# Optimization experiments

Measured on AMD Instinct MI355X. Metric: run time of the kernel, lower is better.

The kernel has to match this reference:

```python
import jax, jax.numpy as jnp
import numpy as np

B, H, N, D, BD, K = 8, 8, 65536, 128, 64, 32


def _l2norm(x, eps=1e-12):
    n = jnp.linalg.norm(x, axis=-1, keepdims=True)
    return x / jnp.maximum(n, eps)


def _topk_sparse_softmax(sim, k):
    # softmax over the top-k entries per (b,h); zeros elsewhere (== masked_fill -inf softmax)
    vals, idx = jax.lax.top_k(sim, k)              # [B,H,k]
    wk = jax.nn.softmax(vals, axis=-1)
    b = jnp.arange(sim.shape[0])[:, None, None]
    h = jnp.arange(sim.shape[1])[None, :, None]
    return jnp.zeros_like(sim).at[b, h, idx].set(wk)  # [B,H,N]


def setup_inputs() -> dict:
    key = jax.random.key(0)
    ks = jax.random.split(key, 14)
    return {
        "memory": jax.random.normal(ks[0], (B, N, D), jnp.float32),
        "read_keys": jax.random.normal(ks[1], (B, H, D), jnp.float32),
        "write_keys": jax.random.normal(ks[2], (B, H, D), jnp.float32),
        "write_vals": jax.random.normal(ks[3], (B, H, D), jnp.float32),
        "erase": jax.random.uniform(ks[4], (B, H), jnp.float32),
        "add_gate": jax.random.uniform(ks[5], (B, H), jnp.float32),
        "beta_r": jax.random.uniform(ks[6], (B, H), jnp.float32),
        "beta_w": jax.random.uniform(ks[7], (B, H), jnp.float32),
        "W_b1": jax.random.normal(ks[8], (D, BD), jnp.float32) * 0.02,
        "b_b1": jnp.zeros((BD,), jnp.float32),
        "W_b2": jax.random.normal(ks[9], (BD, D), jnp.float32) * 0.02,
        "b_b2": jnp.zeros((D,), jnp.float32),
        "W_merge": jax.random.normal(ks[10], (H * D, D), jnp.float32) * 0.02,
        "b_merge": jnp.zeros((D,), jnp.float32),
        "ln_g": jnp.ones((D,), jnp.float32),
        "ln_b": jnp.zeros((D,), jnp.float32),
        "decay_gate": jnp.ones((N,), jnp.float32) * 0.99,
    }


def reference(memory, read_keys, write_keys, write_vals, erase, add_gate,
              beta_r, beta_w, W_b1, b_b1, W_b2, b_b2, W_merge, b_merge,
              ln_g, ln_b, decay_gate):
    # ---- write (erase/add with top-k addressing, head-mean, normalize, decay) ----
    cvals = jax.nn.gelu(write_vals @ W_b1 + b_b1, approximate=False) @ W_b2 + b_b2  # [B,H,D]
    sim_w = jnp.einsum('bhd,bnd->bhn', _l2norm(write_keys), _l2norm(memory)) * beta_w[..., None]
    ww = _topk_sparse_softmax(sim_w, K)                                # [B,H,N]
    # mean_h[mem*(1-w*e)] = mem*(1-mean_h(w*e));  mean_h[w*add*cvals] via einsum/H
    erase_mean = (ww * erase[..., None]).mean(axis=1)                  # [B,N]
    add_part = jnp.einsum('bhn,bhd->bnd', ww * add_gate[..., None], cvals) / H
    mem2 = memory * (1.0 - erase_mean)[..., None] + add_part
    mem2 = _l2norm(mem2 + 1e-8)
    mem2 = mem2 * jax.nn.sigmoid(decay_gate)[None, :, None]            # decay gate

    # ---- read (from updated memory) ----
    sim_r = jnp.einsum('bhd,bnd->bhn', _l2norm(read_keys), _l2norm(mem2)) * beta_r[..., None]
    wr = _topk_sparse_softmax(sim_r, K)
    rph = jnp.einsum('bhn,bnd->bhd', wr, mem2).reshape(mem2.shape[0], H * D)
    merged = rph @ W_merge + b_merge                                   # [B,D]
    mu = merged.mean(axis=-1, keepdims=True)
    var = jnp.mean((merged - mu) ** 2, axis=-1, keepdims=True)
    out = (merged - mu) / jnp.sqrt(var + 1e-5) * ln_g + ln_b           # LayerNorm
    return out
```

## Files before the change

kernel.cpp:

```cpp
#include <hip/hip_runtime.h>
#include <hip/hip_bf16.h>

#define BB   8
#define HH   8
#define NN   65536
#define DD   128
#define BDIM 64
#define KK   32


#define OFF_SIMW 0u
#define OFF_SIMR (OFF_SIMW + 4194304u)
#define OFF_NWK  (OFF_SIMR + 4194304u)
#define OFF_NRK  (OFF_NWK + 8192u)
#define OFF_CV   (OFF_NRK + 8192u)
#define OFF_WIDX (OFF_CV + 8192u)
#define OFF_WVAL (OFF_WIDX + 2048u)
#define OFF_RIDX (OFF_WVAL + 2048u)
#define OFF_RVAL (OFF_RIDX + 2048u)
#define OFF_M2U  (OFF_RVAL + 2048u)
#define OFF_RPH  (OFF_M2U + 262144u)

__device__ __forceinline__ float brsum128(float v, float* sred, int tid) {
  #pragma unroll
  for (int o = 32; o > 0; o >>= 1) v += __shfl_xor(v, o);
  __syncthreads();
  if ((tid & 63) == 0) sred[tid >> 6] = v;
  __syncthreads();
  return sred[0] + sred[1];
}

__global__ __launch_bounds__(128) void k1_setup(
    const float* __restrict__ wkeys, const float* __restrict__ rkeys,
    const float* __restrict__ wvals,
    const float* __restrict__ beta_r, const float* __restrict__ beta_w,
    const float* __restrict__ W_b1, const float* __restrict__ b_b1,
    const float* __restrict__ W_b2, const float* __restrict__ b_b2,
    float* __restrict__ nwk, float* __restrict__ nrk,
    float* __restrict__ cvals, float* __restrict__ rph) {
  int g = blockIdx.x;
  int d = threadIdx.x;
  __shared__ float sred[2];
  __shared__ float wv_s[DD];
  __shared__ float hid[BDIM];

  rph[g * DD + d] = 0.f;

  float wk = wkeys[g * DD + d];
  float rk = rkeys[g * DD + d];
  float wv = wvals[g * DD + d];
  wv_s[d] = wv;

  float s = brsum128(wk * wk, sred, d);
  nwk[g * DD + d] = wk / fmaxf(sqrtf(s), 1e-12f) * beta_w[g];
  s = brsum128(rk * rk, sred, d);
  nrk[g * DD + d] = rk / fmaxf(sqrtf(s), 1e-12f) * beta_r[g];

  __syncthreads();
  if (d < BDIM) {
    float a = b_b1[d];
    #pragma unroll 4
    for (int dd = 0; dd < DD; ++dd) a += wv_s[dd] * W_b1[dd * BDIM + d];
    hid[d] = a * 0.5f * (1.f + erff(a * 0.70710678118654752f));
  }
  __syncthreads();
  float c = b_b2[d];
  #pragma unroll 4
  for (int j = 0; j < BDIM; ++j) c += hid[j] * W_b2[j * DD + d];
  cvals[g * DD + d] = c;
}

__global__ __launch_bounds__(256) void k2_sims(
    const float* __restrict__ mem,
    const float* __restrict__ nwk, const float* __restrict__ nrk,
    float* __restrict__ simw, float* __restrict__ simr) {
  int blk = blockIdx.x;
  int b   = blk >> 8;
  int n   = ((blk & 255) << 8) + threadIdx.x;
  const float4* rowp = (const float4*)(mem + ((size_t)b * NN + n) * DD);

  float dw[HH] = {0,0,0,0,0,0,0,0};
  float dr[HH] = {0,0,0,0,0,0,0,0};
  float nw = 0.f, nr = 0.f;
  const float* kw = nwk + b * HH * DD;
  const float* kr = nrk + b * HH * DD;

  for (int g = 0; g < 4; ++g) {
    float4 q[8];
    #pragma unroll
    for (int i = 0; i < 8; ++i) q[i] = rowp[g * 8 + i];
    #pragma unroll
    for (int i = 0; i < 8; ++i) {
      float xs[4] = {q[i].x, q[i].y, q[i].z, q[i].w};
      #pragma unroll
      for (int e = 0; e < 4; ++e) {
        float xv = xs[e];
        float xr = xv + 1e-8f;
        nw += xv * xv;
        nr += xr * xr;
        int d = g * 32 + i * 4 + e;
        #pragma unroll
        for (int h = 0; h < HH; ++h) {
          dw[h] += xv * kw[h * DD + d];
          dr[h] += xr * kr[h * DD + d];
        }
      }
    }
  }
  float riw = 1.f / fmaxf(sqrtf(nw), 1e-12f);
  float rir = 1.f / fmaxf(sqrtf(nr), 1e-12f);
  #pragma unroll
  for (int h = 0; h < HH; ++h) {
    simw[(size_t)(b * HH + h) * NN + n] = dw[h] * riw;
    simr[(size_t)(b * HH + h) * NN + n] = dr[h] * rir;
  }
}

#define NBKT 1024
#define MAXC 4096
__global__ __launch_bounds__(256) void k_topk(
    const float* __restrict__ sims, int* __restrict__ oidx, float* __restrict__ oval) {
  int blk = blockIdx.x;
  int tid = threadIdx.x;
  const float*  s  = sims + (size_t)blk * NN;
  const float4* s4 = (const float4*)s;
  __shared__ float redv[256];
  __shared__ unsigned hist[NBKT];
  __shared__ float cv[MAXC];
  __shared__ int   ci[MAXC];
  __shared__ float sM, sm, sscale;
  __shared__ int   sthr, scnt;
  __shared__ float selv[KK];
  __shared__ int   seli[KK];

  float mx = -1e30f, mn = 1e30f;
  #pragma unroll 4
  for (int i = tid; i < NN / 4; i += 256) {
    float4 v = s4[i];
    mx = fmaxf(mx, fmaxf(fmaxf(v.x, v.y), fmaxf(v.z, v.w)));
    mn = fminf(mn, fminf(fminf(v.x, v.y), fminf(v.z, v.w)));
  }
  redv[tid] = mx; __syncthreads();
  for (int st = 128; st > 0; st >>= 1) { if (tid < st) redv[tid] = fmaxf(redv[tid], redv[tid + st]); __syncthreads(); }
  if (tid == 0) sM = redv[0];
  __syncthreads();
  redv[tid] = mn; __syncthreads();
  for (int st = 128; st > 0; st >>= 1) { if (tid < st) redv[tid] = fminf(redv[tid], redv[tid + st]); __syncthreads(); }
  if (tid == 0) {
    sm = redv[0];
    float r = sM - sm;
    sscale = (r > 0.f) ? ((float)NBKT / r) : 0.f;
    scnt = 0;
  }
  for (int i = tid; i < NBKT; i += 256) hist[i] = 0u;
  __syncthreads();

  float m_ = sm, sc_ = sscale;
  #pragma unroll 2
  for (int i = tid; i < NN / 4; i += 256) {
    float4 v = s4[i];
    float xs[4] = {v.x, v.y, v.z, v.w};
    #pragma unroll
    for (int e = 0; e < 4; ++e) {
      int bkt = (int)((xs[e] - m_) * sc_);
      bkt = min(NBKT - 1, max(0, bkt));
      atomicAdd(&hist[bkt], 1u);
    }
  }
  __syncthreads();
  if (tid == 0) {
    unsigned acc = 0; int t = NBKT - 1;
    for (; t >= 0; --t) { acc += hist[t]; if (acc >= KK) break; }
    sthr = (t < 0) ? 0 : t;
  }
  __syncthreads();

  int thr = sthr;
  #pragma unroll 2
  for (int i = tid; i < NN / 4; i += 256) {
    float4 v = s4[i];
    float xs[4] = {v.x, v.y, v.z, v.w};
    #pragma unroll
    for (int e = 0; e < 4; ++e) {
      float vv = xs[e];
      int bkt = (int)((vv - m_) * sc_);
      bkt = min(NBKT - 1, max(0, bkt));
      if (bkt >= thr) {
        int p = atomicAdd(&scnt, 1);
        if (p < MAXC) { cv[p] = vv; ci[p] = i * 4 + e; }
      }
    }
  }
  __syncthreads();
  int nc = min(scnt, MAXC);

  if (tid < 64) {
    for (int k = 0; k < KK; ++k) {
      unsigned long long best = 0ull, lbest = 0ull;
      int lj = -1;
      for (int j = tid; j < nc; j += 64) {
        float v = cv[j];
        unsigned u = __float_as_uint(v);
        u = (u & 0x80000000u) ? ~u : (u | 0x80000000u);
        unsigned long long key = ((unsigned long long)u << 32) | (unsigned)(~(unsigned)ci[j]);
        if (key > lbest) { lbest = key; lj = j; }
      }
      best = lbest;
      #pragma unroll
      for (int o = 32; o > 0; o >>= 1) {
        unsigned long long t = __shfl_xor(best, o);
        if (t > best) best = t;
      }
      if (lbest == best && lj >= 0) cv[lj] = -1e30f;
      if (tid == 0) {
        unsigned u = (unsigned)(best >> 32);
        float v = (u & 0x80000000u) ? __uint_as_float(u & 0x7fffffffu) : __uint_as_float(~u);
        selv[k] = v;
        seli[k] = (int)~(unsigned)(best & 0xffffffffu);
      }
    }
    if (tid == 0) {
      float m0 = selv[0], ssum = 0.f;
      float es[KK];
      #pragma unroll
      for (int k = 0; k < KK; ++k) { es[k] = expf(selv[k] - m0); ssum += es[k]; }
      float inv = 1.f / ssum;
      #pragma unroll
      for (int k = 0; k < KK; ++k) {
        oidx[blk * KK + k] = seli[k];
        oval[blk * KK + k] = es[k] * inv;
      }
    }
  }
}

__global__ __launch_bounds__(128) void k4_write(
    const float* __restrict__ mem, const float* __restrict__ erase,
    const float* __restrict__ adg,
    const int* __restrict__ widx, const float* __restrict__ wval,
    const float* __restrict__ cvals, const float* __restrict__ nrk,
    float* __restrict__ mem2u, float* __restrict__ simr) {
  int b  = blockIdx.x >> 8;
  int sl = blockIdx.x & 255;
  int d  = threadIdx.x;
  __shared__ int   swi[256];
  __shared__ float swv[256];
  __shared__ float sred[2 * 9];

  swi[d]       = widx[b * 256 + d];
  swi[d + 128] = widx[b * 256 + d + 128];
  swv[d]       = wval[b * 256 + d];
  swv[d + 128] = wval[b * 256 + d + 128];
  __syncthreads();

  int n = swi[sl];
  for (int j = 0; j < sl; ++j) if (swi[j] == n) return;

  float E = 0.f, addd = 0.f;
  #pragma unroll
  for (int h = 0; h < HH; ++h) {
    float er = erase[b * HH + h];
    float ag = adg[b * HH + h];
    float aw = 0.f;
    #pragma unroll 4
    for (int k = 0; k < KK; ++k) {
      int j = h * KK + k;
      if (swi[j] == n) { float wv = swv[j]; E += wv * er; aw += wv; }
    }
    addd += aw * ag * cvals[(b * HH + h) * DD + d];
  }
  float mval = mem[((size_t)b * NN + n) * DD + d];
  float v = mval * (1.f - E * 0.125f) + addd * 0.125f + 1e-8f;

  float r[9];
  r[0] = v * v;
  #pragma unroll
  for (int h = 0; h < HH; ++h) r[1 + h] = nrk[(b * HH + h) * DD + d] * v;
  #pragma unroll
  for (int o = 32; o > 0; o >>= 1) {
    #pragma unroll
    for (int i = 0; i < 9; ++i) r[i] += __shfl_xor(r[i], o);
  }
  if ((d & 63) == 0) {
    int w = d >> 6;
    #pragma unroll
    for (int i = 0; i < 9; ++i) sred[w * 9 + i] = r[i];
  }
  __syncthreads();
  float S    = sred[0] + sred[9];
  float rinv = 1.f / fmaxf(sqrtf(S), 1e-12f);
  mem2u[(size_t)(b * 256 + sl) * DD + d] = v * rinv;
  if (d < HH) simr[(size_t)(b * HH + d) * NN + n] = (sred[1 + d] + sred[9 + 1 + d]) * rinv;
}

__global__ __launch_bounds__(128) void k6_gather(
    const float* __restrict__ mem, const float* __restrict__ decay,
    const int* __restrict__ widx, const int* __restrict__ ridx,
    const float* __restrict__ rval, const float* __restrict__ mem2u,
    float* __restrict__ rph) {
  int b   = blockIdx.x >> 8;
  int rem = blockIdx.x & 255;
  int d   = threadIdx.x;
  __shared__ int swi[256];
  __shared__ float sred[2];
  swi[d]       = widx[b * 256 + d];
  swi[d + 128] = widx[b * 256 + d + 128];
  __syncthreads();

  int n   = ridx[b * HH * KK + rem];
  float w = rval[b * HH * KK + rem];
  float sc = 1.f / (1.f + expf(-decay[n]));
  int slot = -1;
  for (int j = 0; j < 256; ++j) if (swi[j] == n) { slot = j; break; }
  float u;
  if (slot >= 0) {
    u = mem2u[(size_t)(b * 256 + slot) * DD + d];
  } else {
    float v = mem[((size_t)b * NN + n) * DD + d] + 1e-8f;
    float S = brsum128(v * v, sred, d);
    u = v / fmaxf(sqrtf(S), 1e-12f);
  }
  int h = rem >> 5;
  atomicAdd(&rph[(b * HH + h) * DD + d], w * sc * u);
}

__global__ __launch_bounds__(512) void k7_merge(
    const float* __restrict__ rph, const float* __restrict__ W_merge,
    const float* __restrict__ b_merge, const float* __restrict__ ln_g,
    const float* __restrict__ ln_b, float* __restrict__ out) {
  int b = blockIdx.x;
  int tid = threadIdx.x;
  int d = tid & 127;
  int p = tid >> 7;
  __shared__ float acc_s[4][DD];
  __shared__ float accf[DD];
  __shared__ float smu, svar;

  float a = 0.f;
  int j0 = p * 256;
  #pragma unroll 4
  for (int j = j0; j < j0 + 256; ++j)
    a += rph[b * HH * DD + j] * W_merge[j * DD + d];
  acc_s[p][d] = a;
  __syncthreads();
  if (tid < DD) accf[d] = b_merge[d] + acc_s[0][d] + acc_s[1][d] + acc_s[2][d] + acc_s[3][d];
  __syncthreads();
  if (tid < 64) {
    float x0 = accf[tid], x1 = accf[tid + 64];
    float s1 = x0 + x1, s2 = x0 * x0 + x1 * x1;
    #pragma unroll
    for (int o = 32; o > 0; o >>= 1) { s1 += __shfl_xor(s1, o); s2 += __shfl_xor(s2, o); }
    if (tid == 0) { smu = s1 * (1.f / DD); svar = s2 * (1.f / DD) - smu * smu; }
  }
  __syncthreads();
  if (tid < DD)
    out[b * DD + d] = (accf[d] - smu) * rsqrtf(svar + 1e-5f) * ln_g[d] + ln_b[d];
}

extern "C" void kernel_launch(void* const* d_in, const int* in_sizes, int n_in,
                              void* d_out, int out_size, void* d_ws, size_t ws_size,
                              hipStream_t stream) {
  const float* memory  = (const float*)d_in[0];
  const float* rkeys   = (const float*)d_in[1];
  const float* wkeys   = (const float*)d_in[2];
  const float* wvals   = (const float*)d_in[3];
  const float* erase   = (const float*)d_in[4];
  const float* adg     = (const float*)d_in[5];
  const float* beta_r  = (const float*)d_in[6];
  const float* beta_w  = (const float*)d_in[7];
  const float* W_b1    = (const float*)d_in[8];
  const float* b_b1    = (const float*)d_in[9];
  const float* W_b2    = (const float*)d_in[10];
  const float* b_b2    = (const float*)d_in[11];
  const float* W_merge = (const float*)d_in[12];
  const float* b_merge = (const float*)d_in[13];
  const float* ln_g    = (const float*)d_in[14];
  const float* ln_b    = (const float*)d_in[15];
  const float* decay   = (const float*)d_in[16];

  float* ws   = (float*)d_ws;
  float* simw = ws + OFF_SIMW;
  float* simr = ws + OFF_SIMR;
  float* nwk  = ws + OFF_NWK;
  float* nrk  = ws + OFF_NRK;
  float* cv   = ws + OFF_CV;
  int*   widx = (int*)(ws + OFF_WIDX);
  float* wval = ws + OFF_WVAL;
  int*   ridx = (int*)(ws + OFF_RIDX);
  float* rval = ws + OFF_RVAL;
  float* m2u  = ws + OFF_M2U;
  float* rph  = ws + OFF_RPH;

  hipLaunchKernelGGL(k1_setup, dim3(BB * HH), dim3(128), 0, stream,
                     wkeys, rkeys, wvals, beta_r, beta_w, W_b1, b_b1, W_b2, b_b2,
                     nwk, nrk, cv, rph);
  hipLaunchKernelGGL(k2_sims, dim3(BB * (NN / 256)), dim3(256), 0, stream,
                     memory, nwk, nrk, simw, simr);
  hipLaunchKernelGGL(k_topk, dim3(BB * HH), dim3(256), 0, stream, simw, widx, wval);
  hipLaunchKernelGGL(k4_write, dim3(BB * 256), dim3(128), 0, stream,
                     memory, erase, adg, widx, wval, cv, nrk, m2u, simr);
  hipLaunchKernelGGL(k_topk, dim3(BB * HH), dim3(256), 0, stream, simr, ridx, rval);
  hipLaunchKernelGGL(k6_gather, dim3(BB * 256), dim3(128), 0, stream,
                     memory, decay, widx, ridx, rval, m2u, rph);
  hipLaunchKernelGGL(k7_merge, dim3(BB), dim3(512), 0, stream,
                     rph, W_merge, b_merge, ln_g, ln_b, (float*)d_out);
}
```

Measured before the change: 628.6 us.

## Replace single-block histogram top-k with two-stage parallel wave-level top-k

The old top-k ran one block per (b,h) row: it scanned 65536 scores three times with shared-memory histogram atomics, then did a serial selection. It becomes two kernels. Stage 1 splits each row over 16 blocks of 4 waves, and each wave picks its local top-32 from 1024 register-held keys by repeated shuffle-max. Stage 2 merges the 2048 candidates per row in one wave and computes the softmax with lane shuffles. This spreads work across far more CUs and removes the atomic histogram passes, at the cost of an extra launch and a small candidate buffer.

```diff
diff --git a/kernel.cpp b/kernel.cpp
--- a/kernel.cpp
+++ b/kernel.cpp
@@ -20,6 +20,16 @@
 #define OFF_RVAL (OFF_RIDX + 2048u)
 #define OFF_M2U  (OFF_RVAL + 2048u)
 #define OFF_RPH  (OFF_M2U + 262144u)
+#define OFF_CANDW (OFF_RPH + 8192u)
+#define OFF_CANDR (OFF_CANDW + 262144u)
+
+__device__ __forceinline__ unsigned ordf(float f) {
+  unsigned u = __float_as_uint(f);
+  return (u & 0x80000000u) ? ~u : (u | 0x80000000u);
+}
+__device__ __forceinline__ float unordf(unsigned u) {
+  return (u & 0x80000000u) ? __uint_as_float(u & 0x7fffffffu) : __uint_as_float(~u);
+}
 
 __device__ __forceinline__ float brsum128(float v, float* sred, int tid) {
   #pragma unroll
@@ -116,121 +126,86 @@
   }
 }
 
-#define NBKT 1024
-#define MAXC 4096
-__global__ __launch_bounds__(256) void k_topk(
-    const float* __restrict__ sims, int* __restrict__ oidx, float* __restrict__ oval) {
-  int blk = blockIdx.x;
-  int tid = threadIdx.x;
-  const float*  s  = sims + (size_t)blk * NN;
-  const float4* s4 = (const float4*)s;
-  __shared__ float redv[256];
-  __shared__ unsigned hist[NBKT];
-  __shared__ float cv[MAXC];
-  __shared__ int   ci[MAXC];
-  __shared__ float sM, sm, sscale;
-  __shared__ int   sthr, scnt;
-  __shared__ float selv[KK];
-  __shared__ int   seli[KK];
-
-  float mx = -1e30f, mn = 1e30f;
-  #pragma unroll 4
-  for (int i = tid; i < NN / 4; i += 256) {
-    float4 v = s4[i];
-    mx = fmaxf(mx, fmaxf(fmaxf(v.x, v.y), fmaxf(v.z, v.w)));
-    mn = fminf(mn, fminf(fminf(v.x, v.y), fminf(v.z, v.w)));
-  }
-  redv[tid] = mx; __syncthreads();
-  for (int st = 128; st > 0; st >>= 1) { if (tid < st) redv[tid] = fmaxf(redv[tid], redv[tid + st]); __syncthreads(); }
-  if (tid == 0) sM = redv[0];
-  __syncthreads();
-  redv[tid] = mn; __syncthreads();
-  for (int st = 128; st > 0; st >>= 1) { if (tid < st) redv[tid] = fminf(redv[tid], redv[tid + st]); __syncthreads(); }
-  if (tid == 0) {
-    sm = redv[0];
-    float r = sM - sm;
-    sscale = (r > 0.f) ? ((float)NBKT / r) : 0.f;
-    scnt = 0;
-  }
-  for (int i = tid; i < NBKT; i += 256) hist[i] = 0u;
-  __syncthreads();
-
-  float m_ = sm, sc_ = sscale;
-  #pragma unroll 2
-  for (int i = tid; i < NN / 4; i += 256) {
-    float4 v = s4[i];
-    float xs[4] = {v.x, v.y, v.z, v.w};
-    #pragma unroll
-    for (int e = 0; e < 4; ++e) {
-      int bkt = (int)((xs[e] - m_) * sc_);
-      bkt = min(NBKT - 1, max(0, bkt));
-      atomicAdd(&hist[bkt], 1u);
+__global__ __launch_bounds__(256) void t_stage1(
+    const float* __restrict__ sims, unsigned long long* __restrict__ cand) {
+  int blk   = blockIdx.x;
+  int g     = blk >> 4;
+  int chunk = blk & 15;
+  int tid   = threadIdx.x;
+  int w     = tid >> 6;
+  int lane  = tid & 63;
+  __shared__ unsigned long long sel[4][KK];
+
+  const float4* s4 = (const float4*)(sims + (size_t)g * NN + chunk * 4096 + w * 1024);
+  unsigned long long keys[16];
+  #pragma unroll
+  for (int i = 0; i < 4; ++i) {
+    float4 q = s4[i * 64 + lane];
+    int base = chunk * 4096 + w * 1024 + (i * 64 + lane) * 4;
+    float xs[4] = {q.x, q.y, q.z, q.w};
+    #pragma unroll
+    for (int e = 0; e < 4; ++e)
+      keys[i * 4 + e] = ((unsigned long long)ordf(xs[e]) << 32)
+                        | (unsigned)(~(unsigned)(base + e));
+  }
+  unsigned live = 0xFFFFu;
+  for (int k = 0; k < KK; ++k) {
+    unsigned long long lbest = 0ull; int lslot = -1;
+    #pragma unroll
+    for (int j = 0; j < 16; ++j)
+      if (((live >> j) & 1u) && keys[j] > lbest) { lbest = keys[j]; lslot = j; }
+    unsigned long long best = lbest;
+    #pragma unroll
+    for (int o = 32; o > 0; o >>= 1) {
+      unsigned long long t = __shfl_xor(best, o);
+      if (t > best) best = t;
     }
-  }
-  __syncthreads();
-  if (tid == 0) {
-    unsigned acc = 0; int t = NBKT - 1;
-    for (; t >= 0; --t) { acc += hist[t]; if (acc >= KK) break; }
-    sthr = (t < 0) ? 0 : t;
-  }
-  __syncthreads();
-
-  int thr = sthr;
-  #pragma unroll 2
-  for (int i = tid; i < NN / 4; i += 256) {
-    float4 v = s4[i];
-    float xs[4] = {v.x, v.y, v.z, v.w};
-    #pragma unroll
-    for (int e = 0; e < 4; ++e) {
-      float vv = xs[e];
-      int bkt = (int)((vv - m_) * sc_);
-      bkt = min(NBKT - 1, max(0, bkt));
-      if (bkt >= thr) {
-        int p = atomicAdd(&scnt, 1);
-        if (p < MAXC) { cv[p] = vv; ci[p] = i * 4 + e; }
-      }
+    if (lbest == best && lslot >= 0) live &= ~(1u << lslot);
+    if (lane == 0) sel[w][k] = best;
+  }
+  __syncthreads();
+  if (lane < KK)
+    cand[(size_t)g * 2048 + (chunk * 4 + w) * KK + lane] = sel[w][lane];
+}
+
+__global__ __launch_bounds__(64) void t_stage2(
+    const unsigned long long* __restrict__ cand,
+    int* __restrict__ oidx, float* __restrict__ oval) {
+  int g    = blockIdx.x;
+  int lane = threadIdx.x;
+  __shared__ unsigned long long sel[KK];
+
+  unsigned long long keys[32];
+  #pragma unroll
+  for (int i = 0; i < 32; ++i) keys[i] = cand[(size_t)g * 2048 + i * 64 + lane];
+
+  unsigned live = 0xFFFFFFFFu;
+  for (int k = 0; k < KK; ++k) {
+    unsigned long long lbest = 0ull; int lslot = -1;
+    #pragma unroll
+    for (int j = 0; j < 32; ++j)
+      if (((live >> j) & 1u) && keys[j] > lbest) { lbest = keys[j]; lslot = j; }
+    unsigned long long best = lbest;
+    #pragma unroll
+    for (int o = 32; o > 0; o >>= 1) {
+      unsigned long long t = __shfl_xor(best, o);
+      if (t > best) best = t;
     }
-  }
-  __syncthreads();
-  int nc = min(scnt, MAXC);
-
-  if (tid < 64) {
-    for (int k = 0; k < KK; ++k) {
-      unsigned long long best = 0ull, lbest = 0ull;
-      int lj = -1;
-      for (int j = tid; j < nc; j += 64) {
-        float v = cv[j];
-        unsigned u = __float_as_uint(v);
-        u = (u & 0x80000000u) ? ~u : (u | 0x80000000u);
-        unsigned long long key = ((unsigned long long)u << 32) | (unsigned)(~(unsigned)ci[j]);
-        if (key > lbest) { lbest = key; lj = j; }
-      }
-      best = lbest;
-      #pragma unroll
-      for (int o = 32; o > 0; o >>= 1) {
-        unsigned long long t = __shfl_xor(best, o);
-        if (t > best) best = t;
-      }
-      if (lbest == best && lj >= 0) cv[lj] = -1e30f;
-      if (tid == 0) {
-        unsigned u = (unsigned)(best >> 32);
-        float v = (u & 0x80000000u) ? __uint_as_float(u & 0x7fffffffu) : __uint_as_float(~u);
-        selv[k] = v;
-        seli[k] = (int)~(unsigned)(best & 0xffffffffu);
-      }
-    }
-    if (tid == 0) {
-      float m0 = selv[0], ssum = 0.f;
-      float es[KK];
-      #pragma unroll
-      for (int k = 0; k < KK; ++k) { es[k] = expf(selv[k] - m0); ssum += es[k]; }
-      float inv = 1.f / ssum;
-      #pragma unroll
-      for (int k = 0; k < KK; ++k) {
-        oidx[blk * KK + k] = seli[k];
-        oval[blk * KK + k] = es[k] * inv;
-      }
-    }
+    if (lbest == best && lslot >= 0) live &= ~(1u << lslot);
+    if (lane == 0) sel[k] = best;
+  }
+  __syncthreads();
+  if (lane < KK) {
+    unsigned long long kk = sel[lane];
+    float v  = unordf((unsigned)(kk >> 32));
+    int idx  = (int)~(unsigned)(kk & 0xffffffffu);
+    float m0 = unordf((unsigned)(sel[0] >> 32));
+    float e  = expf(v - m0);
+    float ss = e;
+    #pragma unroll
+    for (int o = 16; o > 0; o >>= 1) ss += __shfl_xor(ss, o);
+    oidx[g * KK + lane] = idx;
+    oval[g * KK + lane] = e / ss;
   }
 }
 
@@ -390,16 +365,20 @@
   float* rval = ws + OFF_RVAL;
   float* m2u  = ws + OFF_M2U;
   float* rph  = ws + OFF_RPH;
+  unsigned long long* candw = (unsigned long long*)(ws + OFF_CANDW);
+  unsigned long long* candr = (unsigned long long*)(ws + OFF_CANDR);
 
   hipLaunchKernelGGL(k1_setup, dim3(BB * HH), dim3(128), 0, stream,
                      wkeys, rkeys, wvals, beta_r, beta_w, W_b1, b_b1, W_b2, b_b2,
                      nwk, nrk, cv, rph);
   hipLaunchKernelGGL(k2_sims, dim3(BB * (NN / 256)), dim3(256), 0, stream,
                      memory, nwk, nrk, simw, simr);
-  hipLaunchKernelGGL(k_topk, dim3(BB * HH), dim3(256), 0, stream, simw, widx, wval);
+  hipLaunchKernelGGL(t_stage1, dim3(BB * HH * 16), dim3(256), 0, stream, simw, candw);
+  hipLaunchKernelGGL(t_stage2, dim3(BB * HH), dim3(64), 0, stream, candw, widx, wval);
   hipLaunchKernelGGL(k4_write, dim3(BB * 256), dim3(128), 0, stream,
                      memory, erase, adg, widx, wval, cv, nrk, m2u, simr);
-  hipLaunchKernelGGL(k_topk, dim3(BB * HH), dim3(256), 0, stream, simr, ridx, rval);
+  hipLaunchKernelGGL(t_stage1, dim3(BB * HH * 16), dim3(256), 0, stream, simr, candr);
+  hipLaunchKernelGGL(t_stage2, dim3(BB * HH), dim3(64), 0, stream, candr, ridx, rval);
   hipLaunchKernelGGL(k6_gather, dim3(BB * 256), dim3(128), 0, stream,
                      memory, decay, widx, ridx, rval, m2u, rph);
   hipLaunchKernelGGL(k7_merge, dim3(BB), dim3(512), 0, stream,
```

Result: slower. 693.8 us (+10.4%).
